# Optimization experiments

Measured on AMD Instinct MI355X. Metric: run time of the kernel, lower is better.

The kernel has to match this reference:

```python
import jax, jax.numpy as jnp
import numpy as np

B, T, D, K = 256, 256, 32, 4096


def setup_inputs() -> dict:
    key = jax.random.key(0)
    k1, k2 = jax.random.split(key)
    x = jax.random.normal(k1, (B, T, D), dtype=jnp.float32)
    # matches nn.Embedding init: uniform(-1/K, 1/K)
    W = jax.random.uniform(k2, (K, D), dtype=jnp.float32, minval=-1.0 / K, maxval=1.0 / K)
    return {"x": x, "W": W}


def _l2norm(v, eps=1e-12):
    # torch F.normalize: v / max(||v||, eps)
    return v / jnp.maximum(jnp.linalg.norm(v, axis=-1, keepdims=True), eps)


def reference(x, W):
    xn = _l2norm(x)                      # [B,T,D]
    en = _l2norm(W)                      # [K,D]
    # squared euclidean distance (argmin identical to torch.cdist argmin)
    d2 = (jnp.sum(xn * xn, axis=-1, keepdims=True)
          - 2.0 * jnp.einsum('btd,kd->btk', xn, en)
          + jnp.sum(en * en, axis=-1))   # [B,T,K] -- dominant intermediate
    indices = jnp.argmin(d2, axis=-1)    # [B,T]
    quantized = W[indices]               # gather from UNnormalized codebook
    codebook_loss = jnp.mean((quantized - jax.lax.stop_gradient(xn)) ** 2)
    commitment_loss = 0.25 * jnp.mean((jax.lax.stop_gradient(quantized) - xn) ** 2)
    quantize_loss = codebook_loss + commitment_loss
    # straight-through estimator
    quantized_ste = xn + jax.lax.stop_gradient(quantized - xn)
    return quantized_ste, indices, quantize_loss
```

## Files before the change

kernel.cpp:

```cpp
#include <hip/hip_runtime.h>
#include <math.h>

#define D 32
#define BT 65536
#define KCODES 4096
#define IOFF 2097152
#define LOFF 2162688
#define FBIG 3.402823466e+38f
#define GAPTHR 8e-5f
#define RERANK_BLOCKS 1024
#define NKC 4
#define NTILES 64
#define GROUP 2
#define RS 4

typedef __attribute__((ext_vector_type(8))) short bf16x8;
typedef __attribute__((ext_vector_type(4))) float f32x4;

__device__ __forceinline__ float seq_sq32(const float v[D]) {
  float s = 0.f;
#pragma unroll
  for (int i = 0; i < D; ++i) s = __fadd_rn(s, __fmul_rn(v[i], v[i]));
  return s;
}

__device__ __forceinline__ float seq_dot32(const float a[D], const float b[D]) {
  float s = 0.f;
#pragma unroll
  for (int i = 0; i < D; ++i) s = __fadd_rn(s, __fmul_rn(a[i], b[i]));
  return s;
}

__device__ __forceinline__ void strict_norm_row(const float* __restrict__ p,
                                                float v[D], float& vv) {
  float a[D];
#pragma unroll
  for (int i = 0; i < D; ++i) a[i] = p[i];
  float m = fmaxf(__fsqrt_rn(seq_sq32(a)), 1e-12f);
#pragma unroll
  for (int i = 0; i < D; ++i) v[i] = __fdiv_rn(a[i], m);
  vv = seq_sq32(v);
}

__device__ __forceinline__ void fast_norm_row(const float* __restrict__ p,
                                              float v[D]) {
  const float4* p4 = reinterpret_cast<const float4*>(p);
  float4 a[8];
#pragma unroll
  for (int i = 0; i < 8; ++i) a[i] = p4[i];
  float sx = 0.f, sy = 0.f, sz = 0.f, sw = 0.f;
#pragma unroll
  for (int i = 0; i < 8; ++i) {
    sx = fmaf(a[i].x, a[i].x, sx);
    sy = fmaf(a[i].y, a[i].y, sy);
    sz = fmaf(a[i].z, a[i].z, sz);
    sw = fmaf(a[i].w, a[i].w, sw);
  }
  float inv = 1.0f / fmaxf(sqrtf((sx + sy) + (sz + sw)), 1e-12f);
#pragma unroll
  for (int i = 0; i < 8; ++i) {
    v[4*i+0] = a[i].x * inv;  v[4*i+1] = a[i].y * inv;
    v[4*i+2] = a[i].z * inv;  v[4*i+3] = a[i].w * inv;
  }
}

__device__ __forceinline__ unsigned bf16_rne(float v) {
  unsigned u = __float_as_uint(v);
  return (u + 0x7FFFu + ((u >> 16) & 1u)) >> 16;
}

__global__ __launch_bounds__(256)
void vq_prep_codes(const float* __restrict__ W, ushort* __restrict__ e_frag,
                   float* __restrict__ en_s, float* __restrict__ ee_s,
                   int* __restrict__ counter, int* __restrict__ done) {
  const int c = blockIdx.x * 256 + threadIdx.x;
  if (c == 0) { counter[0] = 0; done[0] = 0; }
  if (c >= KCODES) return;
  float es[D], ee;
  strict_norm_row(W + (size_t)c * D, es, ee);
  float4* po = reinterpret_cast<float4*>(en_s + (size_t)c * D);
#pragma unroll
  for (int i = 0; i < 8; ++i)
    po[i] = make_float4(es[4*i+0], es[4*i+1], es[4*i+2], es[4*i+3]);
  ee_s[c] = ee;
  float e[D];
  fast_norm_row(W + (size_t)c * D, e);
  const int g = c >> 4, mm = c & 15;
  const size_t tb = (size_t)g * 1024;
#pragma unroll
  for (int b = 0; b < 4; ++b) {
#pragma unroll
    for (int j = 0; j < 8; ++j) {
      float v = e[8*b + j];
      unsigned hb = bf16_rne(v);
      float hf = __uint_as_float(hb << 16);
      unsigned lb = bf16_rne(v - hf);
      size_t sl = tb + (size_t)(16*b + mm) * 8 + j;
      e_frag[sl] = (ushort)hb;
      e_frag[sl + 512] = (ushort)lb;
    }
  }
}

__global__ __launch_bounds__(256, 4)
void vq_scan(const float* __restrict__ x, const ushort* __restrict__ e_frag,
             float4* __restrict__ partials) {
  const int t = threadIdx.x;
  const int lane = t & 63;
  const int kc = blockIdx.y;
  const int rowbase = blockIdx.x * 256 + (t >> 6) * 64;
  const int n = lane & 15;
  const int khi = (lane >> 4) * 4;
  const int g0 = kc * NTILES;

  bf16x8 bh[RS], bl[RS];
#pragma unroll
  for (int rs = 0; rs < RS; ++rs) {
    const int row = rowbase + rs * 16 + n;
    const float4* pr =
        reinterpret_cast<const float4*>(x + (size_t)row * D + (lane >> 4) * 8);
    float4 v0 = pr[0], v1 = pr[1];
    float s = 0.f;
    s = fmaf(v0.x, v0.x, s); s = fmaf(v0.y, v0.y, s);
    s = fmaf(v0.z, v0.z, s); s = fmaf(v0.w, v0.w, s);
    s = fmaf(v1.x, v1.x, s); s = fmaf(v1.y, v1.y, s);
    s = fmaf(v1.z, v1.z, s); s = fmaf(v1.w, v1.w, s);
    s += __shfl_xor(s, 16);
    s += __shfl_xor(s, 32);
    const float inv = 1.0f / fmaxf(sqrtf(s), 1e-12f);
    float e[8] = { v0.x * inv, v0.y * inv, v0.z * inv, v0.w * inv,
                   v1.x * inv, v1.y * inv, v1.z * inv, v1.w * inv };
#pragma unroll
    for (int j = 0; j < 8; ++j) {
      unsigned hb = bf16_rne(e[j]);
      float hf = __uint_as_float(hb << 16);
      unsigned lb = bf16_rne(e[j] - hf);
      bh[rs][j] = (short)hb;
      bl[rs][j] = (short)lb;
    }
  }

  float best[RS], secT[RS];
  int gbest[RS];
#pragma unroll
  for (int rs = 0; rs < RS; ++rs) {
    best[rs] = -FBIG; secT[rs] = -FBIG; gbest[rs] = 0;
  }

  const ushort* fb = e_frag + ((size_t)g0 << 10) + (size_t)lane * 8;

  bf16x8 AH[GROUP], AL[GROUP], BH[GROUP], BL[GROUP];

  auto ldg = [&](bf16x8* H, bf16x8* L, int grp) {
    const ushort* p = fb + (size_t)grp * (GROUP * 1024);
#pragma unroll
    for (int j = 0; j < GROUP; ++j) {
      H[j] = *reinterpret_cast<const bf16x8*>(p + j * 1024);
      L[j] = *reinterpret_cast<const bf16x8*>(p + j * 1024 + 512);
    }
  };

  auto compute = [&](const bf16x8* H, const bf16x8* L, int grp) {
#pragma unroll
    for (int j = 0; j < GROUP; ++j) {
      const int g = grp * GROUP + j;
#pragma unroll
      for (int rs = 0; rs < RS; ++rs) {
        f32x4 z = { 0.f, 0.f, 0.f, 0.f };
        f32x4 acc = __builtin_amdgcn_mfma_f32_16x16x32_bf16(H[j], bh[rs], z, 0, 0, 0);
        acc = __builtin_amdgcn_mfma_f32_16x16x32_bf16(H[j], bl[rs], acc, 0, 0, 0);
        acc = __builtin_amdgcn_mfma_f32_16x16x32_bf16(L[j], bh[rs], acc, 0, 0, 0);
        float tmax = fmaxf(fmaxf(acc[0], acc[1]), fmaxf(acc[2], acc[3]));
        const bool up = tmax > best[rs];
        secT[rs] = fmaxf(secT[rs], fminf(best[rs], tmax));
        gbest[rs] = up ? g : gbest[rs];
        best[rs] = fmaxf(best[rs], tmax);
      }
    }
  };

  const int NG = NTILES / GROUP;
  ldg(AH, AL, 0);
  for (int grp = 0; grp < NG; grp += 2) {
    ldg(BH, BL, grp + 1);
    compute(AH, AL, grp);
    if (grp + 2 < NG) ldg(AH, AL, grp + 2);
    compute(BH, BL, grp + 1);
  }

#pragma unroll
  for (int rs = 0; rs < RS; ++rs) {
    const ushort* pwt = fb + ((size_t)gbest[rs] << 10);
    bf16x8 H = *reinterpret_cast<const bf16x8*>(pwt);
    bf16x8 L = *reinterpret_cast<const bf16x8*>(pwt + 512);
    f32x4 z = { 0.f, 0.f, 0.f, 0.f };
    f32x4 acc = __builtin_amdgcn_mfma_f32_16x16x32_bf16(H, bh[rs], z, 0, 0, 0);
    acc = __builtin_amdgcn_mfma_f32_16x16x32_bf16(H, bl[rs], acc, 0, 0, 0);
    acc = __builtin_amdgcn_mfma_f32_16x16x32_bf16(L, bh[rs], acc, 0, 0, 0);
    const float s0 = acc[0], s1 = acc[1], s2v = acc[2], s3 = acc[3];
    const float m01 = fmaxf(s0, s1), m23 = fmaxf(s2v, s3);
    const float mn01 = fminf(s0, s1), mn23 = fminf(s2v, s3);
    const float s4 = fmaxf(fminf(m01, m23), (m01 >= m23) ? mn01 : mn23);
    float b = best[rs];
    float sec = fmaxf(secT[rs], s4);
    const int q = (s0 == b) ? 0 : (s1 == b) ? 1 : (s2v == b) ? 2 : 3;
    int ii = (g0 + gbest[rs]) * 16 + khi + q;
#pragma unroll
    for (int st = 16; st <= 32; st <<= 1) {
      float ob = __shfl_xor(b, st);
      float os = __shfl_xor(sec, st);
      int oi = __shfl_xor(ii, st);
      float nb = fmaxf(b, ob);
      float ns = fmaxf(fminf(b, ob), fmaxf(sec, os));
      ii = (ob > b) ? oi : ii;
      b = nb; sec = ns;
    }
    if (lane < 16)
      partials[(size_t)kc * BT + rowbase + rs * 16 + lane] =
          make_float4(b, sec, (float)ii, 0.f);
  }
}

__global__ __launch_bounds__(256)
void vq_merge(const float* __restrict__ x, const float* __restrict__ W,
              const float4* __restrict__ partials, float* __restrict__ out,
              int* __restrict__ list, int* __restrict__ counter,
              float* __restrict__ loss_part, int* __restrict__ done, int nkc) {
  __shared__ float red[256];
  __shared__ int last;
  const int t = threadIdx.x;
  const int r = blockIdx.x * 256 + t;
  float4 p = partials[r];
  float best = p.x, sec = p.y, bif = p.z;
  for (int c = 1; c < nkc; ++c) {
    float4 q = partials[(size_t)c * BT + r];
    if (q.x > best) { sec = fmaxf(best, q.y); best = q.x; bif = q.z; }
    else            { sec = fmaxf(sec, q.x); }
  }
  const int bi = (int)bif;
  out[IOFF + r] = bif;

  float xn[D];
  fast_norm_row(x + (size_t)r * D, xn);
  const float4* pw = reinterpret_cast<const float4*>(W + (size_t)bi * D);
  float4* po = reinterpret_cast<float4*>(out + (size_t)r * D);
  float lx = 0.f, ly = 0.f, lz = 0.f, lw = 0.f;
#pragma unroll
  for (int i = 0; i < 8; ++i) {
    float4 w4 = pw[i];
    float dx = w4.x - xn[4*i+0];
    float dy = w4.y - xn[4*i+1];
    float dz = w4.z - xn[4*i+2];
    float dw = w4.w - xn[4*i+3];
    float4 o;
    o.x = xn[4*i+0] + dx;  o.y = xn[4*i+1] + dy;
    o.z = xn[4*i+2] + dz;  o.w = xn[4*i+3] + dw;
    po[i] = o;
    lx = fmaf(dx, dx, lx);
    ly = fmaf(dy, dy, ly);
    lz = fmaf(dz, dz, lz);
    lw = fmaf(dw, dw, lw);
  }
  float lrow = (lx + ly) + (lz + lw);

  if (best - sec <= GAPTHR) {
    int slot = atomicAdd(counter, 1);
    list[slot] = r;
  }

  red[t] = lrow;
  __syncthreads();
  for (int s = 128; s > 0; s >>= 1) {
    if (t < s) red[t] += red[t + s];
    __syncthreads();
  }
  if (t == 0) {
    atomicExch(&loss_part[blockIdx.x], red[0]);
    __threadfence();
    last = (atomicAdd(done, 1) == 255);
  }
  __syncthreads();
  if (last) {
    __threadfence();
    red[t] = atomicAdd(&loss_part[t], 0.0f);
    __syncthreads();
    for (int s = 128; s > 0; s >>= 1) {
      if (t < s) red[t] += red[t + s];
      __syncthreads();
    }
    if (t == 0) {
      float m = red[0] / 2097152.0f;
      out[LOFF] = m + 0.25f * m;
    }
  }
}

__global__ __launch_bounds__(256)
void vq_rerank_strict(const float* __restrict__ x, const float* __restrict__ W,
                      const float* __restrict__ en_s, const float* __restrict__ ee_s,
                      const int* __restrict__ list, const int* __restrict__ counter,
                      float* __restrict__ out) {
  __shared__ float rbest[256];
  __shared__ int ridx[256];
  const int t = threadIdx.x;
  const int nflag = counter[0];

  for (int li = blockIdx.x; li < nflag; li += gridDim.x) {
    const int r = list[li];
    float xn[D], xx;
    strict_norm_row(x + (size_t)r * D, xn, xx);

    float best = FBIG;
    int bi = 0;
    for (int kk = 0; kk < KCODES / 256; ++kk) {
      const int k = t * (KCODES / 256) + kk;
      float en[D];
      const float4* pe = reinterpret_cast<const float4*>(en_s + (size_t)k * D);
#pragma unroll
      for (int i = 0; i < 8; ++i) {
        float4 e = pe[i];
        en[4*i+0] = e.x; en[4*i+1] = e.y; en[4*i+2] = e.z; en[4*i+3] = e.w;
      }
      float dot = seq_dot32(xn, en);
      float d2 = __fadd_rn(__fsub_rn(xx, __fmul_rn(2.0f, dot)), ee_s[k]);
      if (d2 < best) { best = d2; bi = k; }
    }
    rbest[t] = best; ridx[t] = bi;
    __syncthreads();
    for (int s = 128; s > 0; s >>= 1) {
      if (t < s) {
        float vb = rbest[t + s]; int ib = ridx[t + s];
        if (vb < rbest[t] || (vb == rbest[t] && ib < ridx[t])) {
          rbest[t] = vb; ridx[t] = ib;
        }
      }
      __syncthreads();
    }
    if (t == 0) {
      const int a = ridx[0];
      out[IOFF + r] = (float)a;
      float xnf[D], xxf;
      strict_norm_row(x + (size_t)r * D, xnf, xxf);
      const float* wr = W + (size_t)a * D;
      for (int i = 0; i < D; ++i) {
        float dx = __fsub_rn(wr[i], xnf[i]);
        out[(size_t)r * D + i] = __fadd_rn(xnf[i], dx);
      }
    }
    __syncthreads();
  }
}

extern "C" void kernel_launch(void* const* d_in, const int* in_sizes, int n_in,
                              void* d_out, int out_size, void* d_ws, size_t ws_size,
                              hipStream_t stream) {
  const float* x = (const float*)d_in[0];
  const float* W = (const float*)d_in[1];
  float* out = (float*)d_out;

  char* wsb = (char*)d_ws;
  size_t off = (size_t)NKC * BT * 16;
  float4* partials = (float4*)wsb;
  int* list        = (int*)(wsb + off);    off += (size_t)BT * 4;
  int* counter     = (int*)(wsb + off);
  int* done        = counter + 1;          off += 256;
  float* loss_part = (float*)(wsb + off);  off += 1024;
  float* en_s      = (float*)(wsb + off);  off += (size_t)KCODES * D * 4;
  float* ee_s      = (float*)(wsb + off);  off += (size_t)KCODES * 4;
  ushort* e_frag   = (ushort*)(wsb + off);

  vq_prep_codes<<<KCODES / 256, 256, 0, stream>>>(W, e_frag, en_s, ee_s,
                                                  counter, done);
  vq_scan<<<dim3(BT / 256, NKC), 256, 0, stream>>>(x, e_frag, partials);
  vq_merge<<<BT / 256, 256, 0, stream>>>(x, W, partials, out, list, counter,
                                         loss_part, done, NKC);
  vq_rerank_strict<<<RERANK_BLOCKS, 256, 0, stream>>>(x, W, en_s, ee_s, list,
                                                      counter, out);
}
```

Before: 98.98 us.

## Fuse strict rerank into merge kernel and shrink scan blocks to one wave

The separate rerank kernel and its global flagged-row list and atomic counter are removed. Each merge block now collects its own ambiguous rows in shared memory and reranks them in place after the loss reduction. The scan kernel also moves from 256-thread blocks to 64-thread single-wave blocks with four times as many blocks. This saves a kernel launch and global atomics, but a merge block that holds many flagged rows now serializes their exact reranks, which can lengthen the tail.

```diff
diff --git a/kernel.cpp b/kernel.cpp
--- a/kernel.cpp
+++ b/kernel.cpp
@@ -8,7 +8,6 @@
 #define LOFF 2162688
 #define FBIG 3.402823466e+38f
 #define GAPTHR 8e-5f
-#define RERANK_BLOCKS 1024
 #define NKC 4
 #define NTILES 64
 #define GROUP 2
@@ -72,9 +71,9 @@
 __global__ __launch_bounds__(256)
 void vq_prep_codes(const float* __restrict__ W, ushort* __restrict__ e_frag,
                    float* __restrict__ en_s, float* __restrict__ ee_s,
-                   int* __restrict__ counter, int* __restrict__ done) {
+                   int* __restrict__ done) {
   const int c = blockIdx.x * 256 + threadIdx.x;
-  if (c == 0) { counter[0] = 0; done[0] = 0; }
+  if (c == 0) done[0] = 0;
   if (c >= KCODES) return;
   float es[D], ee;
   strict_norm_row(W + (size_t)c * D, es, ee);
@@ -102,13 +101,12 @@
   }
 }
 
-__global__ __launch_bounds__(256, 4)
+__global__ __launch_bounds__(64, 4)
 void vq_scan(const float* __restrict__ x, const ushort* __restrict__ e_frag,
              float4* __restrict__ partials) {
-  const int t = threadIdx.x;
-  const int lane = t & 63;
+  const int lane = threadIdx.x;
   const int kc = blockIdx.y;
-  const int rowbase = blockIdx.x * 256 + (t >> 6) * 64;
+  const int rowbase = blockIdx.x * 64;
   const int n = lane & 15;
   const int khi = (lane >> 4) * 4;
   const int g0 = kc * NTILES;
@@ -224,12 +222,17 @@
 __global__ __launch_bounds__(256)
 void vq_merge(const float* __restrict__ x, const float* __restrict__ W,
               const float4* __restrict__ partials, float* __restrict__ out,
-              int* __restrict__ list, int* __restrict__ counter,
+              const float* __restrict__ en_s, const float* __restrict__ ee_s,
               float* __restrict__ loss_part, int* __restrict__ done, int nkc) {
   __shared__ float red[256];
+  __shared__ int ridx[256];
+  __shared__ int flist[256];
+  __shared__ int fcount;
   __shared__ int last;
   const int t = threadIdx.x;
   const int r = blockIdx.x * 256 + t;
+  if (t == 0) fcount = 0;
+
   float4 p = partials[r];
   float best = p.x, sec = p.y, bif = p.z;
   for (int c = 1; c < nkc; ++c) {
@@ -264,8 +267,8 @@
   float lrow = (lx + ly) + (lz + lw);
 
   if (best - sec <= GAPTHR) {
-    int slot = atomicAdd(counter, 1);
-    list[slot] = r;
+    int s = atomicAdd(&fcount, 1);
+    flist[s] = r;
   }
 
   red[t] = lrow;
@@ -293,25 +296,16 @@
       out[LOFF] = m + 0.25f * m;
     }
   }
-}
-
-__global__ __launch_bounds__(256)
-void vq_rerank_strict(const float* __restrict__ x, const float* __restrict__ W,
-                      const float* __restrict__ en_s, const float* __restrict__ ee_s,
-                      const int* __restrict__ list, const int* __restrict__ counter,
-                      float* __restrict__ out) {
-  __shared__ float rbest[256];
-  __shared__ int ridx[256];
-  const int t = threadIdx.x;
-  const int nflag = counter[0];
-
-  for (int li = blockIdx.x; li < nflag; li += gridDim.x) {
-    const int r = list[li];
-    float xn[D], xx;
-    strict_norm_row(x + (size_t)r * D, xn, xx);
-
-    float best = FBIG;
-    int bi = 0;
+  __syncthreads();
+
+  const int nf = fcount;
+  for (int li = 0; li < nf; ++li) {
+    const int rr = flist[li];
+    float xn2[D], xx2;
+    strict_norm_row(x + (size_t)rr * D, xn2, xx2);
+
+    float bb = FBIG;
+    int bi2 = 0;
     for (int kk = 0; kk < KCODES / 256; ++kk) {
       const int k = t * (KCODES / 256) + kk;
       float en[D];
@@ -321,30 +315,30 @@
         float4 e = pe[i];
         en[4*i+0] = e.x; en[4*i+1] = e.y; en[4*i+2] = e.z; en[4*i+3] = e.w;
       }
-      float dot = seq_dot32(xn, en);
-      float d2 = __fadd_rn(__fsub_rn(xx, __fmul_rn(2.0f, dot)), ee_s[k]);
-      if (d2 < best) { best = d2; bi = k; }
-    }
-    rbest[t] = best; ridx[t] = bi;
+      float dot = seq_dot32(xn2, en);
+      float d2 = __fadd_rn(__fsub_rn(xx2, __fmul_rn(2.0f, dot)), ee_s[k]);
+      if (d2 < bb) { bb = d2; bi2 = k; }
+    }
+    red[t] = bb; ridx[t] = bi2;
     __syncthreads();
     for (int s = 128; s > 0; s >>= 1) {
       if (t < s) {
-        float vb = rbest[t + s]; int ib = ridx[t + s];
-        if (vb < rbest[t] || (vb == rbest[t] && ib < ridx[t])) {
-          rbest[t] = vb; ridx[t] = ib;
+        float vb = red[t + s]; int ib = ridx[t + s];
+        if (vb < red[t] || (vb == red[t] && ib < ridx[t])) {
+          red[t] = vb; ridx[t] = ib;
         }
       }
       __syncthreads();
     }
     if (t == 0) {
       const int a = ridx[0];
-      out[IOFF + r] = (float)a;
+      out[IOFF + rr] = (float)a;
       float xnf[D], xxf;
-      strict_norm_row(x + (size_t)r * D, xnf, xxf);
+      strict_norm_row(x + (size_t)rr * D, xnf, xxf);
       const float* wr = W + (size_t)a * D;
       for (int i = 0; i < D; ++i) {
         float dx = __fsub_rn(wr[i], xnf[i]);
-        out[(size_t)r * D + i] = __fadd_rn(xnf[i], dx);
+        out[(size_t)rr * D + i] = __fadd_rn(xnf[i], dx);
       }
     }
     __syncthreads();
@@ -361,19 +355,14 @@
   char* wsb = (char*)d_ws;
   size_t off = (size_t)NKC * BT * 16;
   float4* partials = (float4*)wsb;
-  int* list        = (int*)(wsb + off);    off += (size_t)BT * 4;
-  int* counter     = (int*)(wsb + off);
-  int* done        = counter + 1;          off += 256;
+  int* done        = (int*)(wsb + off);    off += 256;
   float* loss_part = (float*)(wsb + off);  off += 1024;
   float* en_s      = (float*)(wsb + off);  off += (size_t)KCODES * D * 4;
   float* ee_s      = (float*)(wsb + off);  off += (size_t)KCODES * 4;
   ushort* e_frag   = (ushort*)(wsb + off);
 
-  vq_prep_codes<<<KCODES / 256, 256, 0, stream>>>(W, e_frag, en_s, ee_s,
-                                                  counter, done);
-  vq_scan<<<dim3(BT / 256, NKC), 256, 0, stream>>>(x, e_frag, partials);
-  vq_merge<<<BT / 256, 256, 0, stream>>>(x, W, partials, out, list, counter,
+  vq_prep_codes<<<KCODES / 256, 256, 0, stream>>>(W, e_frag, en_s, ee_s, done);
+  vq_scan<<<dim3(BT / 64, NKC), 64, 0, stream>>>(x, e_frag, partials);
+  vq_merge<<<BT / 256, 256, 0, stream>>>(x, W, partials, out, en_s, ee_s,
                                          loss_part, done, NKC);
-  vq_rerank_strict<<<RERANK_BLOCKS, 256, 0, stream>>>(x, W, en_s, ee_s, list,
-                                                      counter, out);
-}
+}
```

Result: slower. 132.7 us (+34.1%).

## Switch codebook scan from 16x16x32 to 32x32x16 bf16 MFMA tiles

Applied to the files above, without the earlier changes.

Reorganizes the split-bf16 distance scan to use 32x32x16 MFMA instructions, with 32 rows and 32 codes per tile, instead of 16x16x32. The codebook fragment layout in the prep kernel is rewritten to match, and the per-row argmax/second-best tracking and final lane reduction are adjusted accordingly. The aim is better operand reuse, with fewer codebook fragment loads and fewer reduction steps per MAC. In exchange each tile needs more accumulator registers, which may lower occupancy, and the max reduction over 16 accumulator values costs more per tile.

```diff
diff --git a/kernel.cpp b/kernel.cpp
--- a/kernel.cpp
+++ b/kernel.cpp
@@ -10,12 +10,10 @@
 #define GAPTHR 8e-5f
 #define RERANK_BLOCKS 1024
 #define NKC 4
-#define NTILES 64
-#define GROUP 2
-#define RS 4
+#define NT32 32
 
 typedef __attribute__((ext_vector_type(8))) short bf16x8;
-typedef __attribute__((ext_vector_type(4))) float f32x4;
+typedef __attribute__((ext_vector_type(16))) float f32x16;
 
 __device__ __forceinline__ float seq_sq32(const float v[D]) {
   float s = 0.f;
@@ -85,20 +83,19 @@
   ee_s[c] = ee;
   float e[D];
   fast_norm_row(W + (size_t)c * D, e);
-  const int g = c >> 4, mm = c & 15;
-  const size_t tb = (size_t)g * 1024;
-#pragma unroll
-  for (int b = 0; b < 4; ++b) {
-#pragma unroll
-    for (int j = 0; j < 8; ++j) {
-      float v = e[8*b + j];
-      unsigned hb = bf16_rne(v);
-      float hf = __uint_as_float(hb << 16);
-      unsigned lb = bf16_rne(v - hf);
-      size_t sl = tb + (size_t)(16*b + mm) * 8 + j;
-      e_frag[sl] = (ushort)hb;
-      e_frag[sl + 512] = (ushort)lb;
-    }
+  const int g = c >> 5, m = c & 31;
+  const size_t tb = (size_t)g * 2048;
+#pragma unroll
+  for (int d = 0; d < D; ++d) {
+    float v = e[d];
+    unsigned hb = bf16_rne(v);
+    float hf = __uint_as_float(hb << 16);
+    unsigned lb = bf16_rne(v - hf);
+    const int khalf = d >> 4, sub = (d >> 3) & 1, j = d & 7;
+    const int lane = m + 32 * sub;
+    size_t sl = tb + (size_t)khalf * 512 + (size_t)lane * 8 + j;
+    e_frag[sl] = (ushort)hb;
+    e_frag[sl + 1024] = (ushort)lb;
   }
 }
 
@@ -109,114 +106,129 @@
   const int lane = t & 63;
   const int kc = blockIdx.y;
   const int rowbase = blockIdx.x * 256 + (t >> 6) * 64;
-  const int n = lane & 15;
-  const int khi = (lane >> 4) * 4;
-  const int g0 = kc * NTILES;
-
-  bf16x8 bh[RS], bl[RS];
-#pragma unroll
-  for (int rs = 0; rs < RS; ++rs) {
-    const int row = rowbase + rs * 16 + n;
-    const float4* pr =
-        reinterpret_cast<const float4*>(x + (size_t)row * D + (lane >> 4) * 8);
-    float4 v0 = pr[0], v1 = pr[1];
+  const int n = lane & 31;
+  const int kb8 = (lane >> 5) * 8;
+  const int g0t = kc * NT32;
+
+  bf16x8 Bh[2][2], Bl[2][2];
+  float inv_[2];
+#pragma unroll
+  for (int rg = 0; rg < 2; ++rg) {
+    const int row = rowbase + rg * 32 + n;
+    const float* pr = x + (size_t)row * D;
+    float e[2][8];
     float s = 0.f;
-    s = fmaf(v0.x, v0.x, s); s = fmaf(v0.y, v0.y, s);
-    s = fmaf(v0.z, v0.z, s); s = fmaf(v0.w, v0.w, s);
-    s = fmaf(v1.x, v1.x, s); s = fmaf(v1.y, v1.y, s);
-    s = fmaf(v1.z, v1.z, s); s = fmaf(v1.w, v1.w, s);
-    s += __shfl_xor(s, 16);
+#pragma unroll
+    for (int kh = 0; kh < 2; ++kh) {
+      const float4* p4 = reinterpret_cast<const float4*>(pr + kh * 16 + kb8);
+      float4 v0 = p4[0], v1 = p4[1];
+      e[kh][0] = v0.x; e[kh][1] = v0.y; e[kh][2] = v0.z; e[kh][3] = v0.w;
+      e[kh][4] = v1.x; e[kh][5] = v1.y; e[kh][6] = v1.z; e[kh][7] = v1.w;
+#pragma unroll
+      for (int j = 0; j < 8; ++j) s = fmaf(e[kh][j], e[kh][j], s);
+    }
     s += __shfl_xor(s, 32);
     const float inv = 1.0f / fmaxf(sqrtf(s), 1e-12f);
-    float e[8] = { v0.x * inv, v0.y * inv, v0.z * inv, v0.w * inv,
-                   v1.x * inv, v1.y * inv, v1.z * inv, v1.w * inv };
-#pragma unroll
-    for (int j = 0; j < 8; ++j) {
-      unsigned hb = bf16_rne(e[j]);
-      float hf = __uint_as_float(hb << 16);
-      unsigned lb = bf16_rne(e[j] - hf);
-      bh[rs][j] = (short)hb;
-      bl[rs][j] = (short)lb;
-    }
-  }
-
-  float best[RS], secT[RS];
-  int gbest[RS];
-#pragma unroll
-  for (int rs = 0; rs < RS; ++rs) {
-    best[rs] = -FBIG; secT[rs] = -FBIG; gbest[rs] = 0;
-  }
-
-  const ushort* fb = e_frag + ((size_t)g0 << 10) + (size_t)lane * 8;
-
-  bf16x8 AH[GROUP], AL[GROUP], BH[GROUP], BL[GROUP];
-
-  auto ldg = [&](bf16x8* H, bf16x8* L, int grp) {
-    const ushort* p = fb + (size_t)grp * (GROUP * 1024);
-#pragma unroll
-    for (int j = 0; j < GROUP; ++j) {
-      H[j] = *reinterpret_cast<const bf16x8*>(p + j * 1024);
-      L[j] = *reinterpret_cast<const bf16x8*>(p + j * 1024 + 512);
-    }
+    inv_[rg] = inv;
+#pragma unroll
+    for (int kh = 0; kh < 2; ++kh) {
+#pragma unroll
+      for (int j = 0; j < 8; ++j) {
+        float v = e[kh][j] * inv;
+        unsigned hb = bf16_rne(v);
+        float hf = __uint_as_float(hb << 16);
+        unsigned lb = bf16_rne(v - hf);
+        Bh[rg][kh][j] = (short)hb;
+        Bl[rg][kh][j] = (short)lb;
+      }
+    }
+  }
+
+  float best[2] = { -FBIG, -FBIG }, secT[2] = { -FBIG, -FBIG };
+  int gbest[2] = { 0, 0 };
+
+  const ushort* fb = e_frag + ((size_t)g0t * 2048) + (size_t)lane * 8;
+
+  bf16x8 A0[4], A1[4];
+
+  auto ldA = [&](bf16x8* A, int tl) {
+    const ushort* p = fb + (size_t)tl * 2048;
+    A[0] = *reinterpret_cast<const bf16x8*>(p);
+    A[1] = *reinterpret_cast<const bf16x8*>(p + 512);
+    A[2] = *reinterpret_cast<const bf16x8*>(p + 1024);
+    A[3] = *reinterpret_cast<const bf16x8*>(p + 1536);
   };
 
-  auto compute = [&](const bf16x8* H, const bf16x8* L, int grp) {
-#pragma unroll
-    for (int j = 0; j < GROUP; ++j) {
-      const int g = grp * GROUP + j;
-#pragma unroll
-      for (int rs = 0; rs < RS; ++rs) {
-        f32x4 z = { 0.f, 0.f, 0.f, 0.f };
-        f32x4 acc = __builtin_amdgcn_mfma_f32_16x16x32_bf16(H[j], bh[rs], z, 0, 0, 0);
-        acc = __builtin_amdgcn_mfma_f32_16x16x32_bf16(H[j], bl[rs], acc, 0, 0, 0);
-        acc = __builtin_amdgcn_mfma_f32_16x16x32_bf16(L[j], bh[rs], acc, 0, 0, 0);
-        float tmax = fmaxf(fmaxf(acc[0], acc[1]), fmaxf(acc[2], acc[3]));
-        const bool up = tmax > best[rs];
-        secT[rs] = fmaxf(secT[rs], fminf(best[rs], tmax));
-        gbest[rs] = up ? g : gbest[rs];
-        best[rs] = fmaxf(best[rs], tmax);
-      }
+  auto compT = [&](const bf16x8* A, int tl) {
+#pragma unroll
+    for (int rg = 0; rg < 2; ++rg) {
+      f32x16 acc;
+#pragma unroll
+      for (int i = 0; i < 16; ++i) acc[i] = 0.f;
+      acc = __builtin_amdgcn_mfma_f32_32x32x16_bf16(A[0], Bh[rg][0], acc, 0, 0, 0);
+      acc = __builtin_amdgcn_mfma_f32_32x32x16_bf16(A[1], Bh[rg][1], acc, 0, 0, 0);
+      acc = __builtin_amdgcn_mfma_f32_32x32x16_bf16(A[0], Bl[rg][0], acc, 0, 0, 0);
+      acc = __builtin_amdgcn_mfma_f32_32x32x16_bf16(A[1], Bl[rg][1], acc, 0, 0, 0);
+      acc = __builtin_amdgcn_mfma_f32_32x32x16_bf16(A[2], Bh[rg][0], acc, 0, 0, 0);
+      acc = __builtin_amdgcn_mfma_f32_32x32x16_bf16(A[3], Bh[rg][1], acc, 0, 0, 0);
+      float m0 = fmaxf(fmaxf(acc[0], acc[1]), fmaxf(acc[2], acc[3]));
+      float m1 = fmaxf(fmaxf(acc[4], acc[5]), fmaxf(acc[6], acc[7]));
+      float m2 = fmaxf(fmaxf(acc[8], acc[9]), fmaxf(acc[10], acc[11]));
+      float m3 = fmaxf(fmaxf(acc[12], acc[13]), fmaxf(acc[14], acc[15]));
+      float tmax = fmaxf(fmaxf(m0, m1), fmaxf(m2, m3));
+      const bool up = tmax > best[rg];
+      secT[rg] = fmaxf(secT[rg], fminf(best[rg], tmax));
+      gbest[rg] = up ? tl : gbest[rg];
+      best[rg] = fmaxf(best[rg], tmax);
     }
   };
 
-  const int NG = NTILES / GROUP;
-  ldg(AH, AL, 0);
-  for (int grp = 0; grp < NG; grp += 2) {
-    ldg(BH, BL, grp + 1);
-    compute(AH, AL, grp);
-    if (grp + 2 < NG) ldg(AH, AL, grp + 2);
-    compute(BH, BL, grp + 1);
-  }
-
-#pragma unroll
-  for (int rs = 0; rs < RS; ++rs) {
-    const ushort* pwt = fb + ((size_t)gbest[rs] << 10);
-    bf16x8 H = *reinterpret_cast<const bf16x8*>(pwt);
-    bf16x8 L = *reinterpret_cast<const bf16x8*>(pwt + 512);
-    f32x4 z = { 0.f, 0.f, 0.f, 0.f };
-    f32x4 acc = __builtin_amdgcn_mfma_f32_16x16x32_bf16(H, bh[rs], z, 0, 0, 0);
-    acc = __builtin_amdgcn_mfma_f32_16x16x32_bf16(H, bl[rs], acc, 0, 0, 0);
-    acc = __builtin_amdgcn_mfma_f32_16x16x32_bf16(L, bh[rs], acc, 0, 0, 0);
-    const float s0 = acc[0], s1 = acc[1], s2v = acc[2], s3 = acc[3];
-    const float m01 = fmaxf(s0, s1), m23 = fmaxf(s2v, s3);
-    const float mn01 = fminf(s0, s1), mn23 = fminf(s2v, s3);
-    const float s4 = fmaxf(fminf(m01, m23), (m01 >= m23) ? mn01 : mn23);
-    float b = best[rs];
-    float sec = fmaxf(secT[rs], s4);
-    const int q = (s0 == b) ? 0 : (s1 == b) ? 1 : (s2v == b) ? 2 : 3;
-    int ii = (g0 + gbest[rs]) * 16 + khi + q;
-#pragma unroll
-    for (int st = 16; st <= 32; st <<= 1) {
-      float ob = __shfl_xor(b, st);
-      float os = __shfl_xor(sec, st);
-      int oi = __shfl_xor(ii, st);
+  ldA(A0, 0);
+  for (int tl = 0; tl < NT32; tl += 2) {
+    ldA(A1, tl + 1);
+    compT(A0, tl);
+    if (tl + 2 < NT32) ldA(A0, tl + 2);
+    compT(A1, tl + 1);
+  }
+
+#pragma unroll
+  for (int rg = 0; rg < 2; ++rg) {
+    bf16x8 A[4];
+    ldA(A, gbest[rg]);
+    f32x16 acc;
+#pragma unroll
+    for (int i = 0; i < 16; ++i) acc[i] = 0.f;
+    acc = __builtin_amdgcn_mfma_f32_32x32x16_bf16(A[0], Bh[rg][0], acc, 0, 0, 0);
+    acc = __builtin_amdgcn_mfma_f32_32x32x16_bf16(A[1], Bh[rg][1], acc, 0, 0, 0);
+    acc = __builtin_amdgcn_mfma_f32_32x32x16_bf16(A[0], Bl[rg][0], acc, 0, 0, 0);
+    acc = __builtin_amdgcn_mfma_f32_32x32x16_bf16(A[1], Bl[rg][1], acc, 0, 0, 0);
+    acc = __builtin_amdgcn_mfma_f32_32x32x16_bf16(A[2], Bh[rg][0], acc, 0, 0, 0);
+    acc = __builtin_amdgcn_mfma_f32_32x32x16_bf16(A[3], Bh[rg][1], acc, 0, 0, 0);
+    float b2 = -FBIG, s2 = -FBIG;
+#pragma unroll
+    for (int i = 0; i < 16; ++i) {
+      float v = acc[i];
+      s2 = fmaxf(s2, fminf(b2, v));
+      b2 = fmaxf(b2, v);
+    }
+    int q = 0;
+#pragma unroll
+    for (int i = 15; i >= 0; --i) q = (acc[i] == b2) ? i : q;
+    const int m = (q & 3) + 8 * (q >> 2) + 4 * (lane >> 5);
+    float b = best[rg];
+    float sec = fmaxf(secT[rg], s2);
+    int ii = (g0t + gbest[rg]) * 32 + m;
+    {
+      float ob = __shfl_xor(b, 32);
+      float os = __shfl_xor(sec, 32);
+      int oi = __shfl_xor(ii, 32);
       float nb = fmaxf(b, ob);
       float ns = fmaxf(fminf(b, ob), fmaxf(sec, os));
       ii = (ob > b) ? oi : ii;
       b = nb; sec = ns;
     }
-    if (lane < 16)
-      partials[(size_t)kc * BT + rowbase + rs * 16 + lane] =
+    if (lane < 32)
+      partials[(size_t)kc * BT + rowbase + rg * 32 + lane] =
           make_float4(b, sec, (float)ii, 0.f);
   }
 }
```

Result: slower. 102.1 us (+3.1%).
